# Performance work log

Hardware: AMD Instinct MI355X
Metric: run time of the kernel (lower is better)

The kernel has to match this reference:

```python
import jax, jax.numpy as jnp
import numpy as np

N, E = 50000, 800000
IN_DIM, OUT_DIM, NHEAD = 256, 64, 4
SLOPE = 0.2
BN_EPS = 1e-5


def setup_inputs() -> dict:
    key = jax.random.key(0)
    ks = jax.random.split(key, 12)
    HD = NHEAD * OUT_DIM
    s = 1.0 / np.sqrt(IN_DIM)
    inp = {
        'feat': jax.random.normal(ks[0], (N, IN_DIM), dtype=jnp.float32),
        'src': jax.random.randint(ks[1], (E,), 0, N, dtype=jnp.int32),
        'dst': jax.random.randint(ks[2], (E,), 0, N, dtype=jnp.int32),
        # GATv2Conv params (DGL: separate src/dst linear, per-head attn vector, output bias)
        'W_src': jax.random.normal(ks[3], (IN_DIM, HD), dtype=jnp.float32) * s,
        'b_src': jnp.zeros((HD,), dtype=jnp.float32),
        'W_dst': jax.random.normal(ks[4], (IN_DIM, HD), dtype=jnp.float32) * s,
        'b_dst': jnp.zeros((HD,), dtype=jnp.float32),
        'attn': jax.random.normal(ks[5], (NHEAD, OUT_DIM), dtype=jnp.float32) * (1.0 / np.sqrt(OUT_DIM)),
        'out_bias': jnp.zeros((HD,), dtype=jnp.float32),
        # trailing fc: Linear(HD -> OUT_DIM) + BatchNorm1d + LeakyReLU (dropout = identity in eval)
        'fc_W': jax.random.normal(ks[6], (HD, OUT_DIM), dtype=jnp.float32) * (1.0 / np.sqrt(HD)),
        'fc_b': jnp.zeros((OUT_DIM,), dtype=jnp.float32),
        'gamma': jnp.ones((OUT_DIM,), dtype=jnp.float32),
        'beta': jnp.zeros((OUT_DIM,), dtype=jnp.float32),
    }
    return inp


def _leaky(x):
    return jnp.where(x >= 0, x, SLOPE * x)


def reference(feat, src, dst, W_src, b_src, W_dst, b_dst, attn, out_bias, fc_W, fc_b, gamma, beta):
    H, D = NHEAD, OUT_DIM
    h_src = (feat @ W_src + b_src).reshape(N, H, D)
    h_dst = (feat @ W_dst + b_dst).reshape(N, H, D)
    # per-edge GATv2 score: attn . LeakyReLU(h_src[u] + h_dst[v])
    hs_e = h_src[src]                                   # [E,H,D]
    e = jnp.einsum('ehd,hd->eh', _leaky(hs_e + h_dst[dst]), attn)  # [E,H]
    # segment softmax over incoming edges of each dst node
    m = jax.ops.segment_max(e, dst, num_segments=N)     # [N,H]
    ex = jnp.exp(e - m[dst])
    denom = jax.ops.segment_sum(ex, dst, num_segments=N)
    a = ex / denom[dst]                                 # [E,H]
    # weighted scatter-add aggregation
    rst = jax.ops.segment_sum(a[:, :, None] * hs_e, dst, num_segments=N)  # [N,H,D]
    rst = rst + out_bias.reshape(H, D)
    # trailing fc + BatchNorm1d (batch stats) + LeakyReLU
    z = rst.reshape(N, H * D) @ fc_W + fc_b
    mu = jnp.mean(z, axis=0)
    var = jnp.var(z, axis=0)
    z = (z - mu) * jax.lax.rsqrt(var + BN_EPS) * gamma + beta
    return _leaky(z)
```

## Files before the change

kernel.cpp:

```cpp
#include <hip/hip_runtime.h>
#include <math.h>

#define N_NODES 50000
#define N_EDGES 800000
#define HD 256
#define OUT_DIM 64
#define NHEAD 4
#define SLOPE 0.2f
#define BN_EPS 1e-5f
#define LOG2E 1.4426950408889634f
#define NTILES 391
#define HIST_BLOCKS 96
#define NGROUPS 49

typedef __attribute__((ext_vector_type(8))) short short8;
typedef __attribute__((ext_vector_type(4))) float float4v;

__device__ __forceinline__ float leaky(float x) { return x >= 0.f ? x : SLOPE * x; }

__device__ __forceinline__ float bf2f(unsigned short u) {
    return __uint_as_float(((unsigned)u) << 16);
}
__device__ __forceinline__ unsigned short f2bf(float f) {
    unsigned u = __float_as_uint(f);
    unsigned r = (u + 0x7fffu + ((u >> 16) & 1u)) >> 16;
    return (unsigned short)r;
}

template <int CTRL>
__device__ __forceinline__ float ror_add(float v) {
    const int r = __builtin_amdgcn_update_dpp(0, __float_as_int(v), CTRL, 0xF, 0xF, true);
    return v + __int_as_float(r);
}
__device__ __forceinline__ float group16_sum(float v) {
    v = ror_add<0x121>(v);
    v = ror_add<0x122>(v);
    v = ror_add<0x124>(v);
    v = ror_add<0x128>(v);
    return v;
}

__global__ __launch_bounds__(256) void prep_kernel(const float* __restrict__ feat,
                                                   const float* __restrict__ W_src,
                                                   const float* __restrict__ W_dst,
                                                   const float* __restrict__ fc_W,
                                                   unsigned short* __restrict__ feat_bf,
                                                   unsigned short* __restrict__ WtS,
                                                   unsigned short* __restrict__ WtD,
                                                   unsigned short* __restrict__ WtF,
                                                   int* __restrict__ cnt2,
                                                   float* __restrict__ sums,
                                                   int* __restrict__ done) {
    const int b = blockIdx.x;
    const int t = threadIdx.x;
    if (b < 12500) {
        const int i = b * 256 + t;
        const float4 v = ((const float4*)feat)[i];
        ushort4 o;
        o.x = f2bf(v.x); o.y = f2bf(v.y); o.z = f2bf(v.z); o.w = f2bf(v.w);
        ((ushort4*)feat_bf)[i] = o;
    } else if (b < 12756) {
        const int n = b - 12500;
        WtS[(size_t)n * 256 + t] = f2bf(W_src[(size_t)t * 256 + n]);
    } else if (b < 13012) {
        const int n = b - 12756;
        WtD[(size_t)n * 256 + t] = f2bf(W_dst[(size_t)t * 256 + n]);
    } else if (b < 13076) {
        const int n = b - 13012;
        WtF[(size_t)n * 256 + t] = f2bf(fc_W[(size_t)t * 64 + n]);
    } else if (b < 13174) {
        const int i = (b - 13076) * 256 + t;
        if (i < 25000) ((int4*)cnt2)[i] = make_int4(0, 0, 0, 0);
    } else {
        if (t < 128) sums[t] = 0.f;
        if (t == 128) done[0] = 0;
    }
}

__global__ __launch_bounds__(256) void proj_kernel(const unsigned short* __restrict__ A,
                                                   const unsigned short* __restrict__ BtS,
                                                   const unsigned short* __restrict__ BtD,
                                                   const float* __restrict__ bS,
                                                   const float* __restrict__ bD,
                                                   unsigned short* __restrict__ CS,
                                                   unsigned short* __restrict__ CD,
                                                   const int* __restrict__ dst,
                                                   int* __restrict__ cnt) {
    __shared__ unsigned short Bs[64 * 256];

    if (blockIdx.x < HIST_BLOCKS) {
        for (int i = blockIdx.x * 256 + threadIdx.x; i < N_EDGES; i += HIST_BLOCKS * 256)
            atomicAdd(&cnt[dst[i]], 1);
        return;
    }

    const int jid  = blockIdx.x - HIST_BLOCKS;
    const int tile = (jid >> 6) * 8 + (jid & 7);
    if (tile >= NTILES) return;
    const int yy   = (jid >> 3) & 7;

    const int t    = threadIdx.x;
    const int w    = t >> 6;
    const int lane = t & 63;
    const int q    = lane >> 4;
    const int l16  = lane & 15;
    const int c0   = (yy & 3) * 64;
    const bool isD = (yy >= 4);

    const unsigned short* Bt   = isD ? BtD : BtS;
    const float*          bias = isD ? bD  : bS;
    unsigned short*       C    = isD ? CD  : CS;

    {
        const int r   = t >> 2;
        const int seg = t & 3;
        const int c   = r >> 4;
        const int L   = r & 15;
        const unsigned short* g = Bt + (size_t)(c0 + r) * 256 + seg * 64;
#pragma unroll
        for (int kk2 = 0; kk2 < 2; ++kk2) {
            const int kk = seg * 2 + kk2;
#pragma unroll
            for (int q2 = 0; q2 < 4; ++q2)
                *(short8*)(&Bs[((c * 8 + kk) * 64 + q2 * 16 + L) * 8]) =
                    *(const short8*)(g + kk2 * 32 + q2 * 8);
        }
    }
    __syncthreads();

    float vb[4];
#pragma unroll
    for (int c = 0; c < 4; ++c) vb[c] = bias[c0 + c * 16 + l16];

    const int m0 = tile * 128;

    int ar0 = m0 + w * 32 + l16;
    int ar1 = ar0 + 16;
    if (ar0 > N_NODES - 1) ar0 = N_NODES - 1;
    if (ar1 > N_NODES - 1) ar1 = N_NODES - 1;
    const unsigned short* Ab0 = A + (size_t)ar0 * 256 + q * 8;
    const unsigned short* Ab1 = A + (size_t)ar1 * 256 + q * 8;
    short8 afr0[8], afr1[8];
#pragma unroll
    for (int kk = 0; kk < 8; ++kk) {
        afr0[kk] = *(const short8*)(Ab0 + kk * 32);
        afr1[kk] = *(const short8*)(Ab1 + kk * 32);
    }

    float4v a0[4] = {}, a1[4] = {};
#pragma unroll
    for (int kk = 0; kk < 8; ++kk) {
        const short8 af0 = afr0[kk];
        const short8 af1 = afr1[kk];
#pragma unroll
        for (int c = 0; c < 4; ++c) {
            const short8 b = *(const short8*)(&Bs[((c * 8 + kk) * 64 + lane) * 8]);
            a0[c] = __builtin_amdgcn_mfma_f32_16x16x32_bf16(af0, b, a0[c], 0, 0, 0);
            a1[c] = __builtin_amdgcn_mfma_f32_16x16x32_bf16(af1, b, a1[c], 0, 0, 0);
        }
    }

#pragma unroll
    for (int c = 0; c < 4; ++c) {
        const int col = c0 + c * 16 + l16;
#pragma unroll
        for (int i = 0; i < 4; ++i) {
            const int r0 = m0 + w * 32 + q * 4 + i;
            const int r1 = r0 + 16;
            if (r0 < N_NODES) C[(size_t)r0 * 256 + col] = f2bf(a0[c][i] + vb[c]);
            if (r1 < N_NODES) C[(size_t)r1 * 256 + col] = f2bf(a1[c][i] + vb[c]);
        }
    }
}

__global__ __launch_bounds__(256) void fc_bn_kernel(const unsigned short* __restrict__ A,
                                                    const unsigned short* __restrict__ Bt,
                                                    const float* __restrict__ bias,
                                                    float* __restrict__ C,
                                                    float* __restrict__ sums,
                                                    int M) {
    const int w    = threadIdx.x >> 6;
    const int lane = threadIdx.x & 63;
    const int q    = lane >> 4;
    const int l16  = lane & 15;
    const int m0   = blockIdx.x * 64;
    const int t    = threadIdx.x;

    __shared__ float ssum[64], ssq[64];
    if (t < 64) { ssum[t] = 0.f; ssq[t] = 0.f; }

    int arow = m0 + w * 16 + l16;
    if (arow > M - 1) arow = M - 1;
    const unsigned short* Ab  = A  + (size_t)arow * 256 + q * 8;
    const unsigned short* Btb = Bt + (size_t)l16 * 256 + q * 8;

    float4v acc[4] = {};

    for (int k0 = 0; k0 < 256; k0 += 32) {
        const short8 af = *(const short8*)(Ab + k0);
#pragma unroll
        for (int c = 0; c < 4; ++c) {
            const short8 bf = *(const short8*)(Btb + (size_t)c * 16 * 256 + k0);
            acc[c] = __builtin_amdgcn_mfma_f32_16x16x32_bf16(af, bf, acc[c], 0, 0, 0);
        }
    }
    __syncthreads();

#pragma unroll
    for (int c = 0; c < 4; ++c) {
        const int col = c * 16 + l16;
        const float b = bias[col];
        float s = 0.f, qq = 0.f;
#pragma unroll
        for (int i = 0; i < 4; ++i) {
            const int r = m0 + w * 16 + q * 4 + i;
            if (r < M) {
                const float v = acc[c][i] + b;
                C[(size_t)r * 64 + col] = v;
                s += v;
                qq += v * v;
            }
        }
        atomicAdd(&ssum[col], s);
        atomicAdd(&ssq[col], qq);
    }
    __syncthreads();
    if (t < 64) {
        atomicAdd(&sums[t], ssum[t]);
        atomicAdd(&sums[64 + t], ssq[t]);
    }
}

__global__ __launch_bounds__(512) void scan_kernel(const int* __restrict__ cnt,
                                                   int* __restrict__ offs,
                                                   int* __restrict__ bsum,
                                                   int* __restrict__ bpre,
                                                   int* __restrict__ done) {
    __shared__ int s[512];
    __shared__ bool amLast;
    const int t = threadIdx.x;
    const int i = blockIdx.x * 512 + t;
    const int v = (i < N_NODES) ? cnt[i] : 0;
    s[t] = v;
    __syncthreads();
    for (int off = 1; off < 512; off <<= 1) {
        const int x = (t >= off) ? s[t - off] : 0;
        __syncthreads();
        s[t] += x;
        __syncthreads();
    }
    if (i < N_NODES) offs[i] = s[t] - v;
    if (t == 511) {
        bsum[blockIdx.x] = s[511];
        __threadfence();
        amLast = (atomicAdd(done, 1) == (int)gridDim.x - 1);
    }
    __syncthreads();
    if (amLast) {
        const int v2 = (t < (int)gridDim.x) ? atomicAdd(&bsum[t], 0) : 0;
        s[t] = v2;
        __syncthreads();
        for (int off = 1; off < 512; off <<= 1) {
            const int x = (t >= off) ? s[t - off] : 0;
            __syncthreads();
            s[t] += x;
            __syncthreads();
        }
        if (t < (int)gridDim.x) bpre[t] = s[t] - v2;
    }
}

__global__ void scatter_kernel(const int* __restrict__ src,
                               const int* __restrict__ dst,
                               const int* __restrict__ offs,
                               const int* __restrict__ bpre,
                               int* __restrict__ cursor,
                               int* __restrict__ srcl) {
    const int i = blockIdx.x * 256 + threadIdx.x;
    if (i < N_EDGES) {
        const int d = dst[i];
        const int p = offs[d] + bpre[d >> 9] + atomicAdd(&cursor[d], 1);
        srcl[p] = src[i];
    }
}

__global__ __launch_bounds__(256) void agg_fused_kernel(const unsigned short* __restrict__ h_src,
                                                        const unsigned short* __restrict__ h_dst,
                                                        const int* __restrict__ srcl,
                                                        const int* __restrict__ offs,
                                                        const int* __restrict__ bpre,
                                                        const float* __restrict__ attn,
                                                        const float* __restrict__ out_bias,
                                                        unsigned short* __restrict__ rst) {
    const int node = blockIdx.x * 4 + (threadIdx.x >> 6);
    const int lane = threadIdx.x & 63;
    const int d4 = lane * 4;

    const int beg = offs[node] + bpre[node >> 9];
    const int end = (node + 1 == N_NODES) ? N_EDGES
                                          : (offs[node + 1] + bpre[(node + 1) >> 9]);

    const uint2 hdu = *(const uint2*)(h_dst + (size_t)node * 256 + d4);
    const float hd0 = __uint_as_float(hdu.x << 16);
    const float hd1 = __uint_as_float(hdu.x & 0xffff0000u);
    const float hd2 = __uint_as_float(hdu.y << 16);
    const float hd3 = __uint_as_float(hdu.y & 0xffff0000u);

    const float4 araw = *(const float4*)(attn + d4);
    const float c10 = araw.x * (0.6f * LOG2E), c20 = araw.x * (0.4f * LOG2E);
    const float c11 = araw.y * (0.6f * LOG2E), c21 = araw.y * (0.4f * LOG2E);
    const float c12 = araw.z * (0.6f * LOG2E), c22 = araw.z * (0.4f * LOG2E);
    const float c13 = araw.w * (0.6f * LOG2E), c23 = araw.w * (0.4f * LOG2E);

    float wsum = 0.f, a0 = 0.f, a1 = 0.f, a2 = 0.f, a3 = 0.f;

#define EDGE_BODY(sreg)                                                          \
    {                                                                            \
        const unsigned short* row = h_src + (size_t)(sreg) * 256;                \
        const uint2 u = *(const uint2*)(row + d4);                               \
        const float r0 = __uint_as_float(u.x << 16);                             \
        const float r1 = __uint_as_float(u.x & 0xffff0000u);                     \
        const float r2 = __uint_as_float(u.y << 16);                             \
        const float r3 = __uint_as_float(u.y & 0xffff0000u);                     \
        const float y0 = r0 + hd0, y1 = r1 + hd1, y2 = r2 + hd2, y3 = r3 + hd3;  \
        float pp = fmaf(c10, y0, c20 * __builtin_fabsf(y0));                     \
        pp = fmaf(c11, y1, fmaf(c21, __builtin_fabsf(y1), pp));                  \
        pp = fmaf(c12, y2, fmaf(c22, __builtin_fabsf(y2), pp));                  \
        pp = fmaf(c13, y3, fmaf(c23, __builtin_fabsf(y3), pp));                  \
        pp = group16_sum(pp);                                                    \
        const float wg = __builtin_amdgcn_exp2f(pp);                             \
        wsum += wg;                                                              \
        a0 = fmaf(wg, r0, a0);                                                   \
        a1 = fmaf(wg, r1, a1);                                                   \
        a2 = fmaf(wg, r2, a2);                                                   \
        a3 = fmaf(wg, r3, a3);                                                   \
    }

    int p = beg;
    const int nfull = (end - beg) >> 2;
    for (int it = 0; it < nfull; ++it, p += 4) {
        const int s0 = __builtin_amdgcn_readfirstlane(srcl[p]);
        const int s1 = __builtin_amdgcn_readfirstlane(srcl[p + 1]);
        const int s2 = __builtin_amdgcn_readfirstlane(srcl[p + 2]);
        const int s3 = __builtin_amdgcn_readfirstlane(srcl[p + 3]);
        EDGE_BODY(s0);
        EDGE_BODY(s1);
        EDGE_BODY(s2);
        EDGE_BODY(s3);
    }
    for (; p < end; ++p) {
        const int s0 = __builtin_amdgcn_readfirstlane(srcl[p]);
        EDGE_BODY(s0);
    }
#undef EDGE_BODY

    const float inv = (wsum > 0.f) ? 1.f / wsum : 0.f;
    const float4 ob = *(const float4*)(out_bias + d4);
    ushort4 o;
    o.x = f2bf(fmaf(a0, inv, ob.x));
    o.y = f2bf(fmaf(a1, inv, ob.y));
    o.z = f2bf(fmaf(a2, inv, ob.z));
    o.w = f2bf(fmaf(a3, inv, ob.w));
    *(ushort4*)(rst + (size_t)node * 256 + d4) = o;
}

__global__ __launch_bounds__(256) void bn_final_kernel(float* __restrict__ z,
                                                       const float* __restrict__ sums,
                                                       const float* __restrict__ gamma,
                                                       const float* __restrict__ beta) {
    const int i = blockIdx.x * 256 + threadIdx.x;
    if (i < N_NODES * 16) {
        const int c4 = (i & 15) * 4;
        float4 v = ((const float4*)z)[i];
        float out[4] = {v.x, v.y, v.z, v.w};
#pragma unroll
        for (int j = 0; j < 4; ++j) {
            const int col = c4 + j;
            const float mu  = sums[col] * (1.f / N_NODES);
            const float var = sums[64 + col] * (1.f / N_NODES) - mu * mu;
            const float sc  = rsqrtf(var + BN_EPS) * gamma[col];
            const float sh  = beta[col] - mu * sc;
            out[j] = leaky(fmaf(out[j], sc, sh));
        }
        ((float4*)z)[i] = make_float4(out[0], out[1], out[2], out[3]);
    }
}

extern "C" void kernel_launch(void* const* d_in, const int* in_sizes, int n_in,
                              void* d_out, int out_size, void* d_ws, size_t ws_size,
                              hipStream_t stream) {
    const float* feat    = (const float*)d_in[0];
    const int*   src     = (const int*)  d_in[1];
    const int*   dst     = (const int*)  d_in[2];
    const float* W_src   = (const float*)d_in[3];
    const float* b_src   = (const float*)d_in[4];
    const float* W_dst   = (const float*)d_in[5];
    const float* b_dst   = (const float*)d_in[6];
    const float* attn    = (const float*)d_in[7];
    const float* out_bias= (const float*)d_in[8];
    const float* fc_W    = (const float*)d_in[9];
    const float* fc_b    = (const float*)d_in[10];
    const float* gamma   = (const float*)d_in[11];
    const float* beta    = (const float*)d_in[12];
    float* z = (float*)d_out;

    char* ws = (char*)d_ws;
    size_t off = 0;
    auto carve = [&](size_t bytes) -> void* {
        void* p = ws + off;
        off = (off + bytes + 255) & ~(size_t)255;
        return p;
    };
    unsigned short* feat_bf = (unsigned short*)carve((size_t)N_NODES * 256 * 2);
    unsigned short* h_src_bf= (unsigned short*)carve((size_t)N_NODES * 256 * 2);
    unsigned short* h_dst_bf= (unsigned short*)carve((size_t)N_NODES * 256 * 2);
    unsigned short* rst_bf  = (unsigned short*)carve((size_t)N_NODES * 256 * 2);
    unsigned short* WtS     = (unsigned short*)carve((size_t)256 * 256 * 2);
    unsigned short* WtD     = (unsigned short*)carve((size_t)256 * 256 * 2);
    unsigned short* WtF     = (unsigned short*)carve((size_t)64 * 256 * 2);
    int*   srcl   = (int*)  carve((size_t)N_EDGES * 4);
    int*   cnt    = (int*)  carve((size_t)2 * N_NODES * 4);
    int*   cursor = cnt + N_NODES;
    int*   offs   = (int*)  carve((size_t)(N_NODES + 1) * 4);
    int*   bsum   = (int*)  carve(128 * 4);
    int*   bpre   = (int*)  carve(128 * 4);
    float* sums   = (float*)carve(128 * 4);
    int*   done   = (int*)  carve(64);

    const int nchunks = (N_NODES + 511) / 512;

    prep_kernel<<<13175, 256, 0, stream>>>(feat, W_src, W_dst, fc_W,
                                           feat_bf, WtS, WtD, WtF, cnt, sums, done);

    proj_kernel<<<HIST_BLOCKS + NGROUPS * 64, 256, 0, stream>>>(
        feat_bf, WtS, WtD, b_src, b_dst, h_src_bf, h_dst_bf, dst, cnt);

    scan_kernel<<<nchunks, 512, 0, stream>>>(cnt, offs, bsum, bpre, done);
    scatter_kernel<<<(N_EDGES + 255) / 256, 256, 0, stream>>>(src, dst, offs, bpre, cursor, srcl);

    agg_fused_kernel<<<N_NODES / 4, 256, 0, stream>>>(h_src_bf, h_dst_bf, srcl, offs, bpre,
                                                      attn, out_bias, rst_bf);

    fc_bn_kernel<<<(N_NODES + 63) / 64, 256, 0, stream>>>(rst_bf, WtF, fc_b, z, sums, N_NODES);

    bn_final_kernel<<<(N_NODES * 16 + 255) / 256, 256, 0, stream>>>(z, sums, gamma, beta);
}
```

Baseline: 327.1 us.

## Swizzle proj LDS tiles, stage output through LDS, batch agg edge reductions

The projection kernel now XOR-swizzles its B-tile layout in LDS to avoid bank conflicts, and stages the bf16 output tile in LDS so each row is written as 16-byte vectors instead of scattered 2-byte stores. The aggregation kernel issues four gathered row loads before any math and reduces the four edge scores together with an inline-asm DPP sequence, aiming to raise memory-level parallelism and shorten dependency chains. It also moves to 512-thread blocks with 8 nodes each. The inline asm relies on a fixed s_nop count for DPP hazards, and the LDS reuse after __syncthreads assumes the Bs buffer is large enough for the per-wave output staging.

```diff
diff --git a/kernel.cpp b/kernel.cpp
--- a/kernel.cpp
+++ b/kernel.cpp
@@ -10,8 +10,8 @@
 #define BN_EPS 1e-5f
 #define LOG2E 1.4426950408889634f
 #define NTILES 391
+#define NGROUPS 49
 #define HIST_BLOCKS 96
-#define NGROUPS 49
 
 typedef __attribute__((ext_vector_type(8))) short short8;
 typedef __attribute__((ext_vector_type(4))) float float4v;
@@ -38,6 +38,28 @@
     v = ror_add<0x124>(v);
     v = ror_add<0x128>(v);
     return v;
+}
+
+__device__ __forceinline__ void group16_sum4(float& v0, float& v1, float& v2, float& v3) {
+    asm volatile(
+        "s_nop 1\n\t"
+        "v_add_f32_dpp %0, %0, %0 row_ror:1 row_mask:0xf bank_mask:0xf\n\t"
+        "v_add_f32_dpp %1, %1, %1 row_ror:1 row_mask:0xf bank_mask:0xf\n\t"
+        "v_add_f32_dpp %2, %2, %2 row_ror:1 row_mask:0xf bank_mask:0xf\n\t"
+        "v_add_f32_dpp %3, %3, %3 row_ror:1 row_mask:0xf bank_mask:0xf\n\t"
+        "v_add_f32_dpp %0, %0, %0 row_ror:2 row_mask:0xf bank_mask:0xf\n\t"
+        "v_add_f32_dpp %1, %1, %1 row_ror:2 row_mask:0xf bank_mask:0xf\n\t"
+        "v_add_f32_dpp %2, %2, %2 row_ror:2 row_mask:0xf bank_mask:0xf\n\t"
+        "v_add_f32_dpp %3, %3, %3 row_ror:2 row_mask:0xf bank_mask:0xf\n\t"
+        "v_add_f32_dpp %0, %0, %0 row_ror:4 row_mask:0xf bank_mask:0xf\n\t"
+        "v_add_f32_dpp %1, %1, %1 row_ror:4 row_mask:0xf bank_mask:0xf\n\t"
+        "v_add_f32_dpp %2, %2, %2 row_ror:4 row_mask:0xf bank_mask:0xf\n\t"
+        "v_add_f32_dpp %3, %3, %3 row_ror:4 row_mask:0xf bank_mask:0xf\n\t"
+        "v_add_f32_dpp %0, %0, %0 row_ror:8 row_mask:0xf bank_mask:0xf\n\t"
+        "v_add_f32_dpp %1, %1, %1 row_ror:8 row_mask:0xf bank_mask:0xf\n\t"
+        "v_add_f32_dpp %2, %2, %2 row_ror:8 row_mask:0xf bank_mask:0xf\n\t"
+        "v_add_f32_dpp %3, %3, %3 row_ror:8 row_mask:0xf bank_mask:0xf"
+        : "+v"(v0), "+v"(v1), "+v"(v2), "+v"(v3));
 }
 
 __global__ __launch_bounds__(256) void prep_kernel(const float* __restrict__ feat,
@@ -119,10 +141,12 @@
         const unsigned short* g = Bt + (size_t)(c0 + r) * 256 + seg * 64;
 #pragma unroll
         for (int kk2 = 0; kk2 < 2; ++kk2) {
-            const int kk = seg * 2 + kk2;
+            const int kk   = seg * 2 + kk2;
+            const int c8kk = c * 8 + kk;
+            const int key  = ((c8kk >> 1) & 3) << 4;
 #pragma unroll
             for (int q2 = 0; q2 < 4; ++q2)
-                *(short8*)(&Bs[((c * 8 + kk) * 64 + q2 * 16 + L) * 8]) =
+                *(short8*)(&Bs[((c8kk * 64 + q2 * 16 + L) * 8) ^ key]) =
                     *(const short8*)(g + kk2 * 32 + q2 * 8);
         }
     }
@@ -147,6 +171,9 @@
         afr1[kk] = *(const short8*)(Ab1 + kk * 32);
     }
 
+    const int la8 = lane * 8;
+    const int lsw[4] = {la8, la8 ^ 16, la8 ^ 32, la8 ^ 48};
+
     float4v a0[4] = {}, a1[4] = {};
 #pragma unroll
     for (int kk = 0; kk < 8; ++kk) {
@@ -154,22 +181,31 @@
         const short8 af1 = afr1[kk];
 #pragma unroll
         for (int c = 0; c < 4; ++c) {
-            const short8 b = *(const short8*)(&Bs[((c * 8 + kk) * 64 + lane) * 8]);
+            const int c8kk = c * 8 + kk;
+            const short8 b = *(const short8*)(&Bs[c8kk * 512 + lsw[(c8kk >> 1) & 3]]);
             a0[c] = __builtin_amdgcn_mfma_f32_16x16x32_bf16(af0, b, a0[c], 0, 0, 0);
             a1[c] = __builtin_amdgcn_mfma_f32_16x16x32_bf16(af1, b, a1[c], 0, 0, 0);
         }
     }
 
+    __syncthreads();
+    unsigned short* Cw = Bs + w * 2304;
 #pragma unroll
     for (int c = 0; c < 4; ++c) {
-        const int col = c0 + c * 16 + l16;
+        const int cl = c * 16 + l16;
 #pragma unroll
         for (int i = 0; i < 4; ++i) {
-            const int r0 = m0 + w * 32 + q * 4 + i;
-            const int r1 = r0 + 16;
-            if (r0 < N_NODES) C[(size_t)r0 * 256 + col] = f2bf(a0[c][i] + vb[c]);
-            if (r1 < N_NODES) C[(size_t)r1 * 256 + col] = f2bf(a1[c][i] + vb[c]);
-        }
+            Cw[(q * 4 + i) * 72 + cl]        = f2bf(a0[c][i] + vb[c]);
+            Cw[(q * 4 + i + 16) * 72 + cl]   = f2bf(a1[c][i] + vb[c]);
+        }
+    }
+#pragma unroll
+    for (int j = 0; j < 4; ++j) {
+        const int rl = j * 8 + (lane >> 3);
+        const short8 v = *(const short8*)(Cw + rl * 72 + (lane & 7) * 8);
+        const int rg = m0 + w * 32 + rl;
+        if (rg < N_NODES)
+            *(short8*)(&C[(size_t)rg * 256 + c0 + (lane & 7) * 8]) = v;
     }
 }
 
@@ -284,7 +320,7 @@
     }
 }
 
-__global__ __launch_bounds__(256) void agg_fused_kernel(const unsigned short* __restrict__ h_src,
+__global__ __launch_bounds__(512) void agg_fused_kernel(const unsigned short* __restrict__ h_src,
                                                         const unsigned short* __restrict__ h_dst,
                                                         const int* __restrict__ srcl,
                                                         const int* __restrict__ offs,
@@ -292,7 +328,7 @@
                                                         const float* __restrict__ attn,
                                                         const float* __restrict__ out_bias,
                                                         unsigned short* __restrict__ rst) {
-    const int node = blockIdx.x * 4 + (threadIdx.x >> 6);
+    const int node = blockIdx.x * 8 + (threadIdx.x >> 6);
     const int lane = threadIdx.x & 63;
     const int d4 = lane * 4;
 
@@ -314,26 +350,18 @@
 
     float wsum = 0.f, a0 = 0.f, a1 = 0.f, a2 = 0.f, a3 = 0.f;
 
-#define EDGE_BODY(sreg)                                                          \
+#define DOT_PP(u, r0, r1, r2, r3, pp)                                            \
+    const float r0 = __uint_as_float(u.x << 16);                                 \
+    const float r1 = __uint_as_float(u.x & 0xffff0000u);                         \
+    const float r2 = __uint_as_float(u.y << 16);                                 \
+    const float r3 = __uint_as_float(u.y & 0xffff0000u);                         \
+    float pp;                                                                    \
     {                                                                            \
-        const unsigned short* row = h_src + (size_t)(sreg) * 256;                \
-        const uint2 u = *(const uint2*)(row + d4);                               \
-        const float r0 = __uint_as_float(u.x << 16);                             \
-        const float r1 = __uint_as_float(u.x & 0xffff0000u);                     \
-        const float r2 = __uint_as_float(u.y << 16);                             \
-        const float r3 = __uint_as_float(u.y & 0xffff0000u);                     \
         const float y0 = r0 + hd0, y1 = r1 + hd1, y2 = r2 + hd2, y3 = r3 + hd3;  \
-        float pp = fmaf(c10, y0, c20 * __builtin_fabsf(y0));                     \
+        pp = fmaf(c10, y0, c20 * __builtin_fabsf(y0));                           \
         pp = fmaf(c11, y1, fmaf(c21, __builtin_fabsf(y1), pp));                  \
         pp = fmaf(c12, y2, fmaf(c22, __builtin_fabsf(y2), pp));                  \
         pp = fmaf(c13, y3, fmaf(c23, __builtin_fabsf(y3), pp));                  \
-        pp = group16_sum(pp);                                                    \
-        const float wg = __builtin_amdgcn_exp2f(pp);                             \
-        wsum += wg;                                                              \
-        a0 = fmaf(wg, r0, a0);                                                   \
-        a1 = fmaf(wg, r1, a1);                                                   \
-        a2 = fmaf(wg, r2, a2);                                                   \
-        a3 = fmaf(wg, r3, a3);                                                   \
     }
 
     int p = beg;
@@ -343,16 +371,38 @@
         const int s1 = __builtin_amdgcn_readfirstlane(srcl[p + 1]);
         const int s2 = __builtin_amdgcn_readfirstlane(srcl[p + 2]);
         const int s3 = __builtin_amdgcn_readfirstlane(srcl[p + 3]);
-        EDGE_BODY(s0);
-        EDGE_BODY(s1);
-        EDGE_BODY(s2);
-        EDGE_BODY(s3);
+        const uint2 u0 = *(const uint2*)(h_src + (size_t)s0 * 256 + d4);
+        const uint2 u1 = *(const uint2*)(h_src + (size_t)s1 * 256 + d4);
+        const uint2 u2 = *(const uint2*)(h_src + (size_t)s2 * 256 + d4);
+        const uint2 u3 = *(const uint2*)(h_src + (size_t)s3 * 256 + d4);
+        DOT_PP(u0, r00, r01, r02, r03, pp0)
+        DOT_PP(u1, r10, r11, r12, r13, pp1)
+        DOT_PP(u2, r20, r21, r22, r23, pp2)
+        DOT_PP(u3, r30, r31, r32, r33, pp3)
+        group16_sum4(pp0, pp1, pp2, pp3);
+        const float wg0 = __builtin_amdgcn_exp2f(pp0);
+        const float wg1 = __builtin_amdgcn_exp2f(pp1);
+        const float wg2 = __builtin_amdgcn_exp2f(pp2);
+        const float wg3 = __builtin_amdgcn_exp2f(pp3);
+        wsum += (wg0 + wg1) + (wg2 + wg3);
+        a0 = fmaf(wg0, r00, fmaf(wg1, r10, fmaf(wg2, r20, fmaf(wg3, r30, a0))));
+        a1 = fmaf(wg0, r01, fmaf(wg1, r11, fmaf(wg2, r21, fmaf(wg3, r31, a1))));
+        a2 = fmaf(wg0, r02, fmaf(wg1, r12, fmaf(wg2, r22, fmaf(wg3, r32, a2))));
+        a3 = fmaf(wg0, r03, fmaf(wg1, r13, fmaf(wg2, r23, fmaf(wg3, r33, a3))));
     }
     for (; p < end; ++p) {
         const int s0 = __builtin_amdgcn_readfirstlane(srcl[p]);
-        EDGE_BODY(s0);
-    }
-#undef EDGE_BODY
+        const uint2 u0 = *(const uint2*)(h_src + (size_t)s0 * 256 + d4);
+        DOT_PP(u0, r00, r01, r02, r03, pp0)
+        pp0 = group16_sum(pp0);
+        const float wg = __builtin_amdgcn_exp2f(pp0);
+        wsum += wg;
+        a0 = fmaf(wg, r00, a0);
+        a1 = fmaf(wg, r01, a1);
+        a2 = fmaf(wg, r02, a2);
+        a3 = fmaf(wg, r03, a3);
+    }
+#undef DOT_PP
 
     const float inv = (wsum > 0.f) ? 1.f / wsum : 0.f;
     const float4 ob = *(const float4*)(out_bias + d4);
@@ -438,7 +488,7 @@
     scan_kernel<<<nchunks, 512, 0, stream>>>(cnt, offs, bsum, bpre, done);
     scatter_kernel<<<(N_EDGES + 255) / 256, 256, 0, stream>>>(src, dst, offs, bpre, cursor, srcl);
 
-    agg_fused_kernel<<<N_NODES / 4, 256, 0, stream>>>(h_src_bf, h_dst_bf, srcl, offs, bpre,
+    agg_fused_kernel<<<N_NODES / 8, 512, 0, stream>>>(h_src_bf, h_dst_bf, srcl, offs, bpre,
                                                       attn, out_bias, rst_bf);
 
     fc_bn_kernel<<<(N_NODES + 63) / 64, 256, 0, stream>>>(rst_bf, WtF, fc_b, z, sums, N_NODES);
```

New measurement: 325.3 us. About the same (-0.5%).
